# Performance work log

Hardware: AMD Instinct MI355X
Metric: run time of the kernel (lower is better)

The kernel has to match this reference:

```python
import jax, jax.numpy as jnp
import numpy as np

ALPHA = 0.15
CLIP = 5.0
EPS = 1e-6
LN_EPS = 1e-5

B, S, D, F = 4, 4096, 2048, 128


def setup_inputs() -> dict:
    key = jax.random.key(0)
    ks = jax.random.split(key, 8)
    sd = lambda fan_in: 1.0 / np.sqrt(fan_in)
    return {
        "x": jax.random.normal(ks[0], (B, S, D), dtype=jnp.float32),
        "Q_w": jax.random.normal(ks[1], (D, F), dtype=jnp.float32) * sd(D),
        "Q_b": jnp.zeros((F,), jnp.float32),
        "K_w": jax.random.normal(ks[2], (D, F), dtype=jnp.float32) * sd(D),
        "K_b": jnp.zeros((F,), jnp.float32),
        "lo_proj_w": jax.random.normal(ks[3], (D, D), dtype=jnp.float32) * sd(D),
        "lo_proj_b": jnp.zeros((D,), jnp.float32),
        "lo_p_w": jax.random.normal(ks[4], (D, F), dtype=jnp.float32) * sd(D),
        "lo_p_b": jnp.zeros((F,), jnp.float32),
        "proj_w": jax.random.normal(ks[5], (F, D), dtype=jnp.float32) * sd(F),
        "proj_b": jnp.zeros((D,), jnp.float32),
        "O_w": jax.random.normal(ks[6], (D // 2, D), dtype=jnp.float32) * sd(D // 2),
        "O_b": jnp.zeros((D,), jnp.float32),
        "ln_gamma": jnp.ones((D,), jnp.float32),
        "ln_beta": jnp.zeros((D,), jnp.float32),
    }


def _ema_over_time(score):
    # score: [B, S, F]; ema[0]=score[0]; ema[t]=a*score[t]+(1-a)*ema[t-1]
    seq = jnp.swapaxes(score, 0, 1)  # [S, B, F]

    def step(prev, x_t):
        new = ALPHA * x_t + (1.0 - ALPHA) * prev
        return new, new

    init = seq[0]
    _, rest = jax.lax.scan(step, init, seq[1:])
    ema_seq = jnp.concatenate([init[None], rest], axis=0)
    return jnp.swapaxes(ema_seq, 0, 1)


def reference(x, Q_w, Q_b, K_w, K_b, lo_proj_w, lo_proj_b, lo_p_w, lo_p_b,
              proj_w, proj_b, O_w, O_b, ln_gamma, ln_beta):
    x_f32 = x.astype(jnp.float32)
    residual = x_f32

    q = x_f32 @ Q_w + Q_b                    # [B,S,128]
    k = x_f32 @ K_w + K_b                    # [B,S,128]
    # Lo: Dense(d_model) -> gelu -> Dense(128)
    v_h = jax.nn.gelu(x_f32 @ lo_proj_w + lo_proj_b)
    V = v_h @ lo_p_w + lo_p_b                # [B,S,128]

    score = jax.nn.sigmoid(q) * jax.nn.sigmoid(k)
    score_ema = _ema_over_time(score)
    mean_last = jnp.mean(score_ema, axis=-1, keepdims=True)
    denom = jnp.maximum(mean_last, EPS)
    score_clipped = jnp.clip(score_ema / denom, -CLIP, CLIP)

    x_comb = score_clipped * V               # [B,S,128]
    out = x_comb @ proj_w + proj_b           # [B,S,D]  (D even -> no pad)
    a, b = jnp.split(out, 2, axis=-1)
    gated = jax.nn.silu(a) * b               # [B,S,D/2]
    out = gated @ O_w + O_b                  # [B,S,D]

    h = out + residual
    mu = jnp.mean(h, axis=-1, keepdims=True)
    var = jnp.var(h, axis=-1, keepdims=True)
    out = (h - mu) * jax.lax.rsqrt(var + LN_EPS) * ln_gamma + ln_beta
    return out.astype(x.dtype)
```

## Files before the change

kernel.cpp:

```cpp
#include <hip/hip_runtime.h>
#include <cstdint>

#define ALPHA_C 0.15f
#define ONE_MINUS_ALPHA 0.85f
#define CLIP_C 5.0f
#define EPS_C 1e-6f
#define LN_EPS_C 1e-5f

#define Bb 4
#define Ss 4096
#define Dd 2048
#define Mtot (Bb * Ss)

typedef __attribute__((ext_vector_type(8))) short bf16x8;
typedef __attribute__((ext_vector_type(4))) float f32x4;

__device__ __forceinline__ short f2bf(float f) {
  union { float f; uint32_t u; } v; v.f = f;
  uint32_t r = v.u + 0x7fffu + ((v.u >> 16) & 1u);
  return (short)(r >> 16);
}
__device__ __forceinline__ float sigf(float x) { return 1.0f / (1.0f + __expf(-x)); }
__device__ __forceinline__ float geluf(float x) {
  const float c = 0.7978845608028654f;
  float x3 = x * x * x;
  return 0.5f * x * (1.0f + tanhf(c * (x + 0.044715f * x3)));
}

__device__ __forceinline__ void load_lds16(const short* g, short* l) {
  __builtin_amdgcn_global_load_lds((__attribute__((address_space(1))) void*)g,
                                   (__attribute__((address_space(3))) void*)l, 16, 0, 0);
}

#define RD_A(KK)                                                                     \
  _Pragma("unroll") for (int m = 0; m < 8; ++m)                                      \
      a[m] = *(const bf16x8*)&Ab[(wr128 + m * 16 + l16) * 64 +                       \
                                 ((((KK) * 4 + quad) ^ key) * 8)];
#define RD_B(KK)                                                                     \
  _Pragma("unroll") for (int n = 0; n < 4; ++n)                                      \
      bfr[KK][n] = *(const bf16x8*)&Bb2[(wc64 + n * 16 + l16) * 64 +                 \
                                        ((((KK) * 4 + quad) ^ key) * 8)];
#define MFMA_PH(KK, NB)                                                              \
  __builtin_amdgcn_s_setprio(1);                                                     \
  _Pragma("unroll") for (int m = 0; m < 8; ++m) {                                    \
    acc[m][NB] = __builtin_amdgcn_mfma_f32_16x16x32_bf16(a[m], bfr[KK][NB],          \
                                                         acc[m][NB], 0, 0, 0);       \
    acc[m][NB + 1] = __builtin_amdgcn_mfma_f32_16x16x32_bf16(a[m], bfr[KK][NB + 1],  \
                                                             acc[m][NB + 1], 0, 0, 0);\
  }                                                                                  \
  __builtin_amdgcn_s_setprio(0);
#define BARF()                                                                       \
  {                                                                                  \
    asm volatile("" ::: "memory");                                                   \
    __builtin_amdgcn_s_barrier();                                                    \
    asm volatile("" ::: "memory");                                                   \
  }
#define STAGE(tt)                                                                    \
  {                                                                                  \
    short* ls = smem + ((tt) & 1) * 32768;                                           \
    const long co = (long)(tt) * 64;                                                 \
    _Pragma("unroll") for (int i = 0; i < 4; ++i)                                    \
        load_lds16(baseA + (long)i * 64 * lda + co, ls + (i * 64 + w * 8) * 64);     \
    _Pragma("unroll") for (int i = 0; i < 4; ++i)                                    \
        load_lds16(baseB + (long)i * 64 * ldb + co,                                  \
                   ls + 16384 + (i * 64 + w * 8) * 64);                              \
  }

template <int MODE>
__global__ __launch_bounds__(512, 2) void gemm256(
    const short* __restrict__ A, const short* __restrict__ Bt, void* __restrict__ out0,
    void* __restrict__ out1, const float* __restrict__ bias, int K, int lda, int ldb,
    int ldc, int nbx) {
  __shared__ short smem[65536];

  const int tid = threadIdx.x;
  const int w = tid >> 6;
  const int lane = tid & 63;
  const int quad = lane >> 4;
  const int l16 = lane & 15;
  const int key = l16 & 7;
  const int wr = w >> 2;
  const int wc = w & 3;
  const int wr128 = wr * 128;
  const int wc64 = wc * 64;

  const int nwg = gridDim.x;
  const int swz = (blockIdx.x & 7) * (nwg >> 3) + (blockIdx.x >> 3);
  const int by = swz / nbx;
  const int bx = swz - by * nbx;
  const int m0 = by * 256;
  const int n0 = bx * 256;

  const int srow = w * 8 + (lane >> 3);
  const int schunk = (lane & 7) ^ (lane >> 3);
  const short* baseA = A + (long)(m0 + srow) * lda + schunk * 8;
  const short* baseB = Bt + (long)(n0 + srow) * ldb + schunk * 8;

  const int NT = K >> 6;

  f32x4 acc[8][4] = {};
  bf16x8 a[8], bfr[2][4];

  STAGE(0);

  for (int t = 0; t < NT; ++t) {
    const short* Ab = smem + (t & 1) * 32768;
    const short* Bb2 = Ab + 16384;
    if (t + 1 < NT) {
      STAGE(t + 1);
      asm volatile("s_waitcnt vmcnt(8)" ::: "memory");
    } else {
      asm volatile("s_waitcnt vmcnt(0)" ::: "memory");
    }
    __builtin_amdgcn_s_barrier();
    asm volatile("" ::: "memory");
    RD_A(0);
    RD_B(0);
    MFMA_PH(0, 0);
    BARF();
    RD_B(1);
    MFMA_PH(0, 2);
    BARF();
    RD_A(1);
    MFMA_PH(1, 0);
    BARF();
    MFMA_PH(1, 2);
    BARF();
  }

#pragma unroll
  for (int m = 0; m < 8; ++m) {
#pragma unroll
    for (int r = 0; r < 4; ++r) {
      const int row = m0 + wr128 + m * 16 + quad * 4 + r;
#pragma unroll
      for (int n = 0; n < 4; ++n) {
        const int col = n0 + wc64 + n * 16 + l16;
        float v = acc[m][n][r] + bias[col];
        if (MODE == 0) {
          ((float*)out0)[(long)row * ldc + col] = v;
        } else {
          if (n0 == 0) {
            float sh = __shfl_xor(v, 1);
            if (!(lane & 1))
              ((float*)out0)[(long)row * 128 + (col >> 1)] = sigf(v) * sigf(sh);
          } else {
            ((short*)out1)[(long)row * 2048 + (col - 256)] = f2bf(geluf(v));
          }
        }
      }
    }
  }
}

#define BM 128
#define BN 128
#define BK 32

template <int MODE>
__global__ __launch_bounds__(256, 4) void gemm_tn(
    const short* __restrict__ A, const short* __restrict__ Bt, void* __restrict__ out0,
    void* __restrict__ out1, const float* __restrict__ bias, int K, int lda, int ldb,
    int ldc, int nbx, long pstride) {
  __shared__ __align__(16) short As[BM * BK];
  __shared__ __align__(16) short Bs[BN * BK];

  const int tid = threadIdx.x;
  const int wave = tid >> 6;
  const int lane = tid & 63;
  const int quad = lane >> 4;
  const int l16 = lane & 15;

  const int bid = blockIdx.x;
  const int panel = bid / (8 * nbx);
  const int rem = bid - panel * (8 * nbx);
  const int by = panel * 8 + (rem & 7);
  const int bx = rem >> 3;
  const int m0 = by * BM;
  const int n0 = bx * BN;
  const int wm = (wave & 1) * 64;
  const int wn = (wave >> 1) * 64;

  if (MODE == 5) {
    A += (long)blockIdx.y * K;
    Bt += (long)blockIdx.y * K;
  }

  const int srow = wave * 32 + (lane >> 2);
  const int skoff = ((lane & 3) ^ ((lane >> 3) & 3)) * 8;
  const short* agp = A + (long)(m0 + srow) * lda + skoff;
  const short* bgp = Bt + (long)(n0 + srow) * ldb + skoff;
  const short* agp2 = agp + (long)16 * lda;
  const short* bgp2 = bgp + (long)16 * ldb;
  short* al = As + (wave * 32) * BK;
  short* al2 = al + 16 * BK;
  short* bl = Bs + (wave * 32) * BK;
  short* bl2 = bl + 16 * BK;

  const int rsw = (l16 >> 1) & 3;

  f32x4 acc[4][4] = {};

  for (int k0 = 0; k0 < K; k0 += BK) {
    __syncthreads();
    load_lds16(agp + k0, al);
    load_lds16(agp2 + k0, al2);
    load_lds16(bgp + k0, bl);
    load_lds16(bgp2 + k0, bl2);
    __syncthreads();

    bf16x8 af[4], bfr[4];
#pragma unroll
    for (int i = 0; i < 4; ++i)
      af[i] = *(const bf16x8*)&As[(wm + i * 16 + l16) * BK + (quad ^ rsw) * 8];
#pragma unroll
    for (int j = 0; j < 4; ++j)
      bfr[j] = *(const bf16x8*)&Bs[(wn + j * 16 + l16) * BK + (quad ^ rsw) * 8];
#pragma unroll
    for (int i = 0; i < 4; ++i)
#pragma unroll
      for (int j = 0; j < 4; ++j)
        acc[i][j] = __builtin_amdgcn_mfma_f32_16x16x32_bf16(af[i], bfr[j], acc[i][j], 0, 0, 0);
  }

#pragma unroll
  for (int i = 0; i < 4; ++i) {
#pragma unroll
    for (int r = 0; r < 4; ++r) {
      const int row = m0 + wm + i * 16 + quad * 4 + r;
#pragma unroll
      for (int j = 0; j < 4; ++j) {
        const int col = n0 + wn + j * 16 + l16;
        float v = acc[i][j][r];
        if (MODE != 5) v += bias[col];
        if (MODE == 0) {
          ((float*)out0)[(long)row * ldc + col] = v;
        } else if (MODE == 5) {
          float* o = (float*)out0 + (long)blockIdx.y * pstride;
          o[(long)row * ldc + col] = v;
        } else if (MODE == 3) {
          if (n0 < 256) {
            float sh = __shfl_xor(v, 1);
            if (!(lane & 1))
              ((float*)out0)[(long)row * 128 + (col >> 1)] = sigf(v) * sigf(sh);
          } else {
            ((short*)out1)[(long)row * 2048 + (col - 256)] = f2bf(geluf(v));
          }
        } else if (MODE == 4) {
          float sh = __shfl_xor(v, 1);
          if (!(lane & 1))
            ((short*)out0)[(long)row * 1024 + (col >> 1)] = f2bf(v * sigf(v) * sh);
        }
      }
    }
  }
}

__global__ __launch_bounds__(256) void cast_x_kernel(const float* __restrict__ in,
                                                     short* __restrict__ out, long n4) {
  long i = (long)blockIdx.x * blockDim.x + threadIdx.x;
  const long stride = (long)gridDim.x * blockDim.x;
  for (; i < n4; i += stride) {
    float4 v = ((const float4*)in)[i];
    short4 o;
    o.x = f2bf(v.x); o.y = f2bf(v.y); o.z = f2bf(v.z); o.w = f2bf(v.w);
    ((short4*)out)[i] = o;
  }
}

template <int MAP>
__global__ __launch_bounds__(256) void tcast_kernel(const float* __restrict__ in,
                                                    short* __restrict__ out, int R, int C) {
  __shared__ float t[32][33];
  const int c0 = blockIdx.x * 32, r0 = blockIdx.y * 32;
  const int tx = threadIdx.x, ty = threadIdx.y;
#pragma unroll
  for (int i = 0; i < 32; i += 8)
    t[ty + i][tx] = in[(long)(r0 + ty + i) * C + (c0 + tx)];
  __syncthreads();
#pragma unroll
  for (int i = 0; i < 32; i += 8) {
    const int c = c0 + ty + i;
    const int orow = (MAP == 0) ? c
                   : (MAP == 1) ? 2 * c
                   : (MAP == 2) ? 2 * c + 1
                                : (c < 1024 ? 2 * c : 2 * (c - 1024) + 1);
    out[(long)orow * R + (r0 + tx)] = f2bf(t[tx][ty + i]);
  }
}

__global__ void pack_bias_kernel(const float* __restrict__ qb, const float* __restrict__ kb,
                                 const float* __restrict__ lob, float* __restrict__ o) {
  int i = blockIdx.x * 256 + threadIdx.x;
  if (i < 256) o[i] = (i & 1) ? kb[i >> 1] : qb[i >> 1];
  else if (i < 2304) o[i] = lob[i - 256];
}
__global__ void pack_pbias_kernel(const float* __restrict__ pjb, float* __restrict__ o) {
  int i = blockIdx.x * 256 + threadIdx.x;
  o[i] = (i & 1) ? pjb[1024 + (i >> 1)] : pjb[i >> 1];
}

#define SEG 64
#define WARM 96
__global__ __launch_bounds__(128) void ema_kernel(const float* __restrict__ score,
                                                  float* __restrict__ ema) {
  const int f = threadIdx.x;
  const int b = blockIdx.y;
  const int seg = blockIdx.x;
  const int t0 = seg * SEG;
  const int tstart = (t0 >= WARM) ? (t0 - WARM) : 0;
  const int tend = t0 + SEG;
  const float* __restrict__ base = score + (long)b * Ss * 128;
  float* __restrict__ eb = ema + (long)b * Ss * 128;

  float e = base[(long)tstart * 128 + f];
  if (seg == 0) eb[f] = e;

  int t = tstart + 1;
  const int CH = 8;
  const int nch = (tend - t) / CH;
  float cur[CH];
#pragma unroll
  for (int i = 0; i < CH; ++i) cur[i] = ALPHA_C * base[(long)(t + i) * 128 + f];
  for (int c = 0; c < nch; ++c) {
    float nxt[CH] = {};
    if (c + 1 < nch) {
#pragma unroll
      for (int i = 0; i < CH; ++i) nxt[i] = ALPHA_C * base[(long)(t + CH + i) * 128 + f];
    }
#pragma unroll
    for (int i = 0; i < CH; ++i) {
      e = fmaf(ONE_MINUS_ALPHA, e, cur[i]);
      const int tt = t + i;
      if (tt >= t0) eb[(long)tt * 128 + f] = e;
    }
#pragma unroll
    for (int i = 0; i < CH; ++i) cur[i] = nxt[i];
    t += CH;
  }
  for (; t < tend; ++t) {
    e = fmaf(ONE_MINUS_ALPHA, e, ALPHA_C * base[(long)t * 128 + f]);
    if (t >= t0) eb[(long)t * 128 + f] = e;
  }
}

__global__ __launch_bounds__(256) void comb_kernel(const float* __restrict__ ema,
                                                   const float* __restrict__ vpart,
                                                   const float* __restrict__ lob,
                                                   short* __restrict__ xcomb) {
  const int wv = threadIdx.x >> 6;
  const int lane = threadIdx.x & 63;
  const long row = (long)blockIdx.x * 4 + wv;
  const float* er = ema + row * 128;
  float e0 = er[lane], e1 = er[lane + 64];
  float s = e0 + e1;
#pragma unroll
  for (int m = 1; m < 64; m <<= 1) s += __shfl_xor(s, m, 64);
  const float denom = fmaxf(s * (1.0f / 128.0f), EPS_C);
  const float inv = 1.0f / denom;
  const float c0 = fminf(fmaxf(e0 * inv, -CLIP_C), CLIP_C);
  const float c1 = fminf(fmaxf(e1 * inv, -CLIP_C), CLIP_C);
  const long PS = (long)Mtot * 128;
  float va = lob[lane], vb = lob[lane + 64];
#pragma unroll
  for (int p = 0; p < 4; ++p) {
    va += vpart[p * PS + row * 128 + lane];
    vb += vpart[p * PS + row * 128 + lane + 64];
  }
  xcomb[row * 128 + lane] = f2bf(c0 * va);
  xcomb[row * 128 + 64 + lane] = f2bf(c1 * vb);
}

__global__ __launch_bounds__(256) void ln_kernel(float* __restrict__ io,
                                                 const float* __restrict__ x,
                                                 const float* __restrict__ gamma,
                                                 const float* __restrict__ beta) {
  const long row = blockIdx.x;
  const int tid = threadIdx.x;
  const int wv = tid >> 6, lane = tid & 63;
  float* rp = io + row * 2048;
  const float* xp = x + row * 2048;
  float4 v0 = ((const float4*)rp)[tid * 2];
  float4 v1 = ((const float4*)rp)[tid * 2 + 1];
  float4 x0 = ((const float4*)xp)[tid * 2];
  float4 x1 = ((const float4*)xp)[tid * 2 + 1];
  float h[8] = {v0.x + x0.x, v0.y + x0.y, v0.z + x0.z, v0.w + x0.w,
                v1.x + x1.x, v1.y + x1.y, v1.z + x1.z, v1.w + x1.w};
  float sum = 0.f, ss = 0.f;
#pragma unroll
  for (int i = 0; i < 8; ++i) { sum += h[i]; ss += h[i] * h[i]; }
#pragma unroll
  for (int m = 1; m < 64; m <<= 1) {
    sum += __shfl_xor(sum, m, 64);
    ss += __shfl_xor(ss, m, 64);
  }
  __shared__ float rs[4], rq[4];
  if (lane == 0) { rs[wv] = sum; rq[wv] = ss; }
  __syncthreads();
  sum = rs[0] + rs[1] + rs[2] + rs[3];
  ss = rq[0] + rq[1] + rq[2] + rq[3];
  const float mu = sum * (1.0f / 2048.0f);
  const float var = ss * (1.0f / 2048.0f) - mu * mu;
  const float rstd = rsqrtf(var + LN_EPS_C);
  const int c0 = tid * 8;
  float o[8];
#pragma unroll
  for (int i = 0; i < 8; ++i)
    o[i] = (h[i] - mu) * rstd * gamma[c0 + i] + beta[c0 + i];
  ((float4*)rp)[tid * 2]     = make_float4(o[0], o[1], o[2], o[3]);
  ((float4*)rp)[tid * 2 + 1] = make_float4(o[4], o[5], o[6], o[7]);
}

extern "C" void kernel_launch(void* const* d_in, const int* in_sizes, int n_in,
                              void* d_out, int out_size, void* d_ws, size_t ws_size,
                              hipStream_t stream) {
  const float* x         = (const float*)d_in[0];
  const float* Q_w       = (const float*)d_in[1];
  const float* Q_b       = (const float*)d_in[2];
  const float* K_w       = (const float*)d_in[3];
  const float* K_b       = (const float*)d_in[4];
  const float* lo_proj_w = (const float*)d_in[5];
  const float* lo_proj_b = (const float*)d_in[6];
  const float* lo_p_w    = (const float*)d_in[7];
  const float* lo_p_b    = (const float*)d_in[8];
  const float* proj_w    = (const float*)d_in[9];
  const float* proj_b    = (const float*)d_in[10];
  const float* O_w       = (const float*)d_in[11];
  const float* O_b       = (const float*)d_in[12];
  const float* ln_g      = (const float*)d_in[13];
  const float* ln_b      = (const float*)d_in[14];

  char* ws = (char*)d_ws;
  size_t off = 0;
  auto alloc = [&](size_t bytes) {
    char* p = ws + off;
    off += (bytes + 255) & ~(size_t)255;
    return p;
  };
  short* x16   = (short*)alloc((size_t)Mtot * Dd * 2);
  short* h16   = (short*)alloc((size_t)Mtot * Dd * 2);
  float* score = (float*)alloc((size_t)Mtot * 128 * 4);
  float* emab  = (float*)alloc((size_t)Mtot * 128 * 4);
  short* xcomb = (short*)alloc((size_t)Mtot * 128 * 2);
  short* gated = (short*)alloc((size_t)Mtot * 1024 * 2);
  short* wbig  = (short*)alloc((size_t)2304 * 2048 * 2);
  short* lpt   = (short*)alloc((size_t)128 * 2048 * 2);
  short* prjt  = (short*)alloc((size_t)2048 * 128 * 2);
  short* ot    = (short*)alloc((size_t)2048 * 1024 * 2);
  float* biasb = (float*)alloc(2304 * 4);
  float* pbias = (float*)alloc(2048 * 4);
  float* vpart = (float*)x16;
  float* outf  = (float*)d_out;

  cast_x_kernel<<<8192, 256, 0, stream>>>(x, x16, (long)Mtot * Dd / 4);
  tcast_kernel<1><<<dim3(4, 64), dim3(32, 8), 0, stream>>>(Q_w, wbig, 2048, 128);
  tcast_kernel<2><<<dim3(4, 64), dim3(32, 8), 0, stream>>>(K_w, wbig, 2048, 128);
  tcast_kernel<0><<<dim3(64, 64), dim3(32, 8), 0, stream>>>(lo_proj_w, wbig + 256 * 2048, 2048, 2048);
  tcast_kernel<0><<<dim3(4, 64), dim3(32, 8), 0, stream>>>(lo_p_w, lpt, 2048, 128);
  tcast_kernel<3><<<dim3(64, 4), dim3(32, 8), 0, stream>>>(proj_w, prjt, 128, 2048);
  tcast_kernel<0><<<dim3(64, 32), dim3(32, 8), 0, stream>>>(O_w, ot, 1024, 2048);
  pack_bias_kernel<<<9, 256, 0, stream>>>(Q_b, K_b, lo_proj_b, biasb);
  pack_pbias_kernel<<<8, 256, 0, stream>>>(proj_b, pbias);

  gemm256<3><<<576, 512, 0, stream>>>(x16, wbig, score, h16, biasb,
                                      2048, 2048, 2048, 0, 9);
  ema_kernel<<<dim3(Ss / SEG, 4), 128, 0, stream>>>(score, emab);
  gemm_tn<5><<<dim3(128, 4), 256, 0, stream>>>(h16, lpt, vpart, nullptr, nullptr,
                                               512, 2048, 2048, 128, 1, (long)Mtot * 128);
  comb_kernel<<<Mtot / 4, 256, 0, stream>>>(emab, vpart, lo_p_b, xcomb);
  gemm_tn<4><<<16 * 128, 256, 0, stream>>>(xcomb, prjt, gated, nullptr, pbias,
                                           128, 128, 128, 1024, 16, 0);
  gemm256<0><<<512, 512, 0, stream>>>(gated, ot, outf, nullptr, O_b,
                                      1024, 1024, 1024, 2048, 8);
  ln_kernel<<<Mtot, 256, 0, stream>>>(outf, x, ln_g, ln_b);
}
```

Before: 745.8 us.

## Restructure GEMM main loop into quarter-phases with interleaved half-tile staging

Rewrites the 256x256 bf16 GEMM main loop. Global-to-LDS staging of the next K-tile is split into four half-tile loads spread across the four MFMA phases, and A/B fragments are reloaded per 4x4 quadrant so fewer registers stay live. The loop is unrolled by two so the LDS buffer index is a compile-time constant. The aim is to smooth memory traffic, overlap it better with MFMA work and lower register pressure, at the cost of more LDS reads, extra lgkmcnt waits and extra barriers per tile.

```diff
diff --git a/kernel.cpp b/kernel.cpp
--- a/kernel.cpp
+++ b/kernel.cpp
@@ -32,22 +32,21 @@
                                    (__attribute__((address_space(3))) void*)l, 16, 0, 0);
 }
 
-#define RD_A(KK)                                                                     \
-  _Pragma("unroll") for (int m = 0; m < 8; ++m)                                      \
-      a[m] = *(const bf16x8*)&Ab[(wr128 + m * 16 + l16) * 64 +                       \
-                                 ((((KK) * 4 + quad) ^ key) * 8)];
+
+#define RD_A(MH, KK)                                                                 \
+  _Pragma("unroll") for (int mm = 0; mm < 4; ++mm)                                   \
+      a[mm] = *(const bf16x8*)&Ab[(wr128 + ((MH) * 4 + mm) * 16 + l16) * 64 +        \
+                                  ((((KK) * 4 + quad) ^ key) * 8)];
 #define RD_B(KK)                                                                     \
-  _Pragma("unroll") for (int n = 0; n < 4; ++n)                                      \
-      bfr[KK][n] = *(const bf16x8*)&Bb2[(wc64 + n * 16 + l16) * 64 +                 \
-                                        ((((KK) * 4 + quad) ^ key) * 8)];
-#define MFMA_PH(KK, NB)                                                              \
+  _Pragma("unroll") for (int nn = 0; nn < 4; ++nn)                                   \
+      bq[nn] = *(const bf16x8*)&Bl[(wc64 + nn * 16 + l16) * 64 +                     \
+                                   ((((KK) * 4 + quad) ^ key) * 8)];
+#define MFMA_Q(MH)                                                                   \
   __builtin_amdgcn_s_setprio(1);                                                     \
-  _Pragma("unroll") for (int m = 0; m < 8; ++m) {                                    \
-    acc[m][NB] = __builtin_amdgcn_mfma_f32_16x16x32_bf16(a[m], bfr[KK][NB],          \
-                                                         acc[m][NB], 0, 0, 0);       \
-    acc[m][NB + 1] = __builtin_amdgcn_mfma_f32_16x16x32_bf16(a[m], bfr[KK][NB + 1],  \
-                                                             acc[m][NB + 1], 0, 0, 0);\
-  }                                                                                  \
+  _Pragma("unroll") for (int mm = 0; mm < 4; ++mm)                                   \
+  _Pragma("unroll") for (int nn = 0; nn < 4; ++nn)                                   \
+      acc[(MH) * 4 + mm][nn] = __builtin_amdgcn_mfma_f32_16x16x32_bf16(              \
+          a[mm], bq[nn], acc[(MH) * 4 + mm][nn], 0, 0, 0);                           \
   __builtin_amdgcn_s_setprio(0);
 #define BARF()                                                                       \
   {                                                                                  \
@@ -55,15 +54,61 @@
     __builtin_amdgcn_s_barrier();                                                    \
     asm volatile("" ::: "memory");                                                   \
   }
-#define STAGE(tt)                                                                    \
+#define STAGE_HALF_A(TT, H)                                                          \
   {                                                                                  \
-    short* ls = smem + ((tt) & 1) * 32768;                                           \
-    const long co = (long)(tt) * 64;                                                 \
-    _Pragma("unroll") for (int i = 0; i < 4; ++i)                                    \
-        load_lds16(baseA + (long)i * 64 * lda + co, ls + (i * 64 + w * 8) * 64);     \
-    _Pragma("unroll") for (int i = 0; i < 4; ++i)                                    \
-        load_lds16(baseB + (long)i * 64 * ldb + co,                                  \
-                   ls + 16384 + (i * 64 + w * 8) * 64);                              \
+    short* ls = smem + ((TT) & 1) * 32768 + (H) * 8192;                              \
+    const long co = (long)(TT) * 64;                                                 \
+    load_lds16(baseA + ((H) * 128 + 0) * (long)lda + co, ls + w * 512);              \
+    load_lds16(baseA + ((H) * 128 + 64) * (long)lda + co, ls + 4096 + w * 512);      \
+  }
+#define STAGE_HALF_B(TT, H)                                                          \
+  {                                                                                  \
+    short* ls = smem + ((TT) & 1) * 32768 + 16384 + (H) * 8192;                      \
+    const long co = (long)(TT) * 64;                                                 \
+    load_lds16(baseB + ((H) * 128 + 0) * (long)ldb + co, ls + w * 512);              \
+    load_lds16(baseB + ((H) * 128 + 64) * (long)ldb + co, ls + 4096 + w * 512);      \
+  }
+
+#define TILE_BODY(CB, STG, TN)                                                       \
+  {                                                                                  \
+    const short* Ab = smem + (CB) * 32768;                                           \
+    const short* Bl = Ab + 16384;                                                    \
+                                                                  \
+    if (STG) {                                                                       \
+      STAGE_HALF_A(TN, 0);                                                           \
+      asm volatile("s_waitcnt vmcnt(2)" ::: "memory");                               \
+    } else {                                                                         \
+      asm volatile("s_waitcnt vmcnt(0)" ::: "memory");                               \
+    }                                                                                \
+    __builtin_amdgcn_s_barrier();                                                    \
+    asm volatile("" ::: "memory");                                                   \
+    RD_A(0, 0);                                                                      \
+    RD_B(0);                                                                         \
+    asm volatile("s_waitcnt lgkmcnt(0)" ::: "memory");                               \
+    MFMA_Q(0);                                                                       \
+    BARF();                                                                          \
+                                                                        \
+    RD_A(1, 0);                                                                      \
+    if (STG) STAGE_HALF_A(TN, 1);                                                    \
+    __builtin_amdgcn_s_barrier();                                                    \
+    asm volatile("s_waitcnt lgkmcnt(0)" ::: "memory");                               \
+    MFMA_Q(1);                                                                       \
+    BARF();                                                                          \
+                                                                        \
+    RD_A(0, 1);                                                                      \
+    RD_B(1);                                                                         \
+    if (STG) STAGE_HALF_B(TN, 0);                                                    \
+    __builtin_amdgcn_s_barrier();                                                    \
+    asm volatile("s_waitcnt lgkmcnt(0)" ::: "memory");                               \
+    MFMA_Q(0);                                                                       \
+    BARF();                                                                          \
+                                                                        \
+    RD_A(1, 1);                                                                      \
+    if (STG) STAGE_HALF_B(TN, 1);                                                    \
+    __builtin_amdgcn_s_barrier();                                                    \
+    asm volatile("s_waitcnt lgkmcnt(0)" ::: "memory");                               \
+    MFMA_Q(1);                                                                       \
+    BARF();                                                                          \
   }
 
 template <int MODE>
@@ -91,42 +136,28 @@
   const int m0 = by * 256;
   const int n0 = bx * 256;
 
-  const int srow = w * 8 + (lane >> 3);
-  const int schunk = (lane & 7) ^ (lane >> 3);
-  const short* baseA = A + (long)(m0 + srow) * lda + schunk * 8;
-  const short* baseB = Bt + (long)(n0 + srow) * ldb + schunk * 8;
+  const int rowoff = lane >> 3;
+  const int schunk = ((lane & 7) ^ (lane >> 3)) * 8;
+  const short* baseA = A + (long)(m0 + w * 8 + rowoff) * lda + schunk;
+  const short* baseB = Bt + (long)(n0 + w * 8 + rowoff) * ldb + schunk;
 
   const int NT = K >> 6;
 
   f32x4 acc[8][4] = {};
-  bf16x8 a[8], bfr[2][4];
-
-  STAGE(0);
-
-  for (int t = 0; t < NT; ++t) {
-    const short* Ab = smem + (t & 1) * 32768;
-    const short* Bb2 = Ab + 16384;
-    if (t + 1 < NT) {
-      STAGE(t + 1);
-      asm volatile("s_waitcnt vmcnt(8)" ::: "memory");
-    } else {
-      asm volatile("s_waitcnt vmcnt(0)" ::: "memory");
-    }
-    __builtin_amdgcn_s_barrier();
-    asm volatile("" ::: "memory");
-    RD_A(0);
-    RD_B(0);
-    MFMA_PH(0, 0);
-    BARF();
-    RD_B(1);
-    MFMA_PH(0, 2);
-    BARF();
-    RD_A(1);
-    MFMA_PH(1, 0);
-    BARF();
-    MFMA_PH(1, 2);
-    BARF();
-  }
+  bf16x8 a[4], bq[4];
+
+  STAGE_HALF_A(0, 0);
+  STAGE_HALF_A(0, 1);
+  STAGE_HALF_B(0, 0);
+  STAGE_HALF_B(0, 1);
+
+  int t = 0;
+  for (; t < NT - 2; t += 2) {
+    TILE_BODY(0, 1, t + 1);
+    TILE_BODY(1, 1, t + 2);
+  }
+  TILE_BODY(0, 1, t + 1);
+  TILE_BODY(1, 0, 0);
 
 #pragma unroll
   for (int m = 0; m < 8; ++m) {
```

Result: faster. 721.1 us (-3.3%).
